# Performance work log

Measured on AMD Instinct MI355X. Metric: run time of the kernel, lower is better.

Reference implementation:

```python
import jax, jax.numpy as jnp
import numpy as np

DIL = 2  # dilation of the 3x3 neighborhood (hardcoded in the torch module)
# 8 non-center neighbor offsets of a dilated 3x3 kernel
_OFFSETS = [(-DIL, -DIL), (-DIL, 0), (-DIL, DIL),
            (0, -DIL),              (0, DIL),
            (DIL, -DIL), (DIL, 0),  (DIL, DIL)]


def setup_inputs() -> dict:
    key = jax.random.key(0)
    k1, k2 = jax.random.split(key)
    shape = (16, 1, 1024, 1024)
    y_true = jax.random.uniform(k1, shape, dtype=jnp.float32)
    y_pred = jax.random.uniform(k2, shape, dtype=jnp.float32)
    return {"y_true": y_true, "y_pred": y_pred}


def reference(y_true, y_pred):
    # --- BCE with torch's log clamp at -100 (reduction='none') ---
    log_p  = jnp.maximum(jnp.log(y_pred),   -100.0)
    log_1p = jnp.maximum(jnp.log1p(-y_pred), -100.0)
    a = -(y_true * log_p + (1.0 - y_true) * log_1p)

    # --- detached copy (y_pred.clone().detach()) ---
    sloss = jax.lax.stop_gradient(y_pred)

    # --- max |center - neighbor| over 8 dilated neighbors, zero-padded borders ---
    H, W = sloss.shape[2], sloss.shape[3]
    padded = jnp.pad(sloss, ((0, 0), (0, 0), (DIL, DIL), (DIL, DIL)))
    unfolded_weights = jnp.zeros_like(sloss)
    for dy, dx in _OFFSETS:
        nb = padded[:, :, DIL + dy:DIL + dy + H, DIL + dx:DIL + dx + W]
        unfolded_weights = jnp.maximum(unfolded_weights, jnp.abs(sloss - nb))

    # thred[thred < 0.5] = 0; loss1 uses thred BEFORE the >=0.5 -> 1 assignment
    thred = jnp.where(sloss >= 0.5, sloss, 0.0)
    loss = unfolded_weights * thred + a
    return loss.mean()
```

## Files before the change

kernel.cpp:

```cpp
#include <hip/hip_runtime.h>

#define HH 1024
#define WW 1024
#define NB 16
#define TR 8
#define SR (TR + 4)
#define NBLK (NB * (HH / TR))
#define NELEM ((long long)NB * HH * WW)

__device__ __forceinline__ void lds_win(const float* __restrict__ S, int row,
                                        int c0, bool ledge, bool redge, float w[8]) {
    const float* p = S + row * WW;
    float2 L = *(const float2*)(p + (ledge ? c0 : c0 - 2));
    float4 M = *(const float4*)(p + c0);
    float2 R = *(const float2*)(p + (redge ? c0 : c0 + 4));
    if (ledge) { L.x = 0.f; L.y = 0.f; }
    if (redge) { R.x = 0.f; R.y = 0.f; }
    w[0]=L.x; w[1]=L.y; w[2]=M.x; w[3]=M.y; w[4]=M.z; w[5]=M.w; w[6]=R.x; w[7]=R.y;
}

__global__ __launch_bounds__(512) void closs_main(const float* __restrict__ yt,
                                                  const float* __restrict__ yp,
                                                  float* __restrict__ partial) {
    __shared__ float S[SR * WW];

    const int bid   = blockIdx.x;
    const int img   = bid >> 7;
    const int tile  = bid & 127;
    const int y0    = tile * TR;
    const int tid   = threadIdx.x;
    const int lane  = tid & 255;
    const int rhalf = tid >> 8;
    const int c0    = lane << 2;

    const float* __restrict__ ybase = yp + (long long)img * (HH * WW);
    const float* __restrict__ tbase = yt + ((long long)img * HH + y0) * WW;

#pragma unroll
    for (int ii = 0; ii < 6; ++ii) {
        const int r  = (ii << 1) + rhalf;
        const int gy = y0 - 2 + r;
        float4 v = make_float4(0.f, 0.f, 0.f, 0.f);
        if (gy >= 0 && gy < HH)
            v = *(const float4*)(ybase + gy * WW + c0);
        *(float4*)&S[r * WW + c0] = v;
    }
    __syncthreads();

    const bool ledge = (lane == 0);
    const bool redge = (lane == 255);
    const int  kb    = rhalf << 2;

    float sum = 0.f;
#pragma unroll
    for (int k2 = 0; k2 < 4; ++k2) {
        const int k = kb + k2;
        float A[8], B[8], C[8];
        lds_win(S, k,     c0, ledge, redge, A);
        lds_win(S, k + 2, c0, ledge, redge, B);
        lds_win(S, k + 4, c0, ledge, redge, C);

        const float4 t4 = *(const float4*)(tbase + k * WW + c0);
        const float tt[4] = {t4.x, t4.y, t4.z, t4.w};

#pragma unroll
        for (int j = 0; j < 4; ++j) {
            const float c = B[j + 2];
            const float mxA = fmaxf(fmaxf(A[j], A[j + 2]), A[j + 4]);
            const float mxB = fmaxf(B[j], B[j + 4]);
            const float mxC = fmaxf(fmaxf(C[j], C[j + 2]), C[j + 4]);
            const float mx  = fmaxf(fmaxf(mxA, mxB), mxC);
            const float mnA = fminf(fminf(A[j], A[j + 2]), A[j + 4]);
            const float mnB = fminf(B[j], B[j + 4]);
            const float mnC = fminf(fminf(C[j], C[j + 2]), C[j + 4]);
            const float mn  = fminf(fminf(mnA, mnB), mnC);
            const float w   = fmaxf(mx - c, c - mn);

            const float lp  = fmaxf(__logf(c), -100.f);
            const float l1p = fmaxf(__logf(1.f - c), -100.f);
            const float th  = (c >= 0.5f) ? c : 0.f;
            sum += w * th - l1p - tt[j] * (lp - l1p);
        }
    }

    for (int o = 32; o > 0; o >>= 1) sum += __shfl_down(sum, o);
    __shared__ float wsum[8];
    if ((tid & 63) == 0) wsum[tid >> 6] = sum;
    __syncthreads();
    if (tid == 0) {
        float t = 0.f;
#pragma unroll
        for (int i = 0; i < 8; ++i) t += wsum[i];
        partial[bid] = t;
    }
}

__global__ __launch_bounds__(1024) void closs_reduce(const float* __restrict__ partial,
                                                     float* __restrict__ out) {
    const float2* p2 = (const float2*)partial;
    float2 v = p2[threadIdx.x];
    float s = v.x + v.y;
    for (int o = 32; o > 0; o >>= 1) s += __shfl_down(s, o);
    __shared__ float wsum[16];
    if ((threadIdx.x & 63) == 0) wsum[threadIdx.x >> 6] = s;
    __syncthreads();
    if (threadIdx.x == 0) {
        float t = 0.f;
#pragma unroll
        for (int i = 0; i < 16; ++i) t += wsum[i];
        out[0] = t * (1.0f / (float)NELEM);
    }
}

extern "C" void kernel_launch(void* const* d_in, const int* in_sizes, int n_in,
                              void* d_out, int out_size, void* d_ws, size_t ws_size,
                              hipStream_t stream) {
    const float* y_true = (const float*)d_in[0];
    const float* y_pred = (const float*)d_in[1];
    float* out = (float*)d_out;
    float* partial = (float*)d_ws;

    closs_main<<<NBLK, 512, 0, stream>>>(y_true, y_pred, partial);
    closs_reduce<<<1, 1024, 0, stream>>>(partial, out);
}
```

Baseline: 144.8 us.

## Double tile height and prefetch second-half rows during first-half compute

```diff
diff --git a/kernel.cpp b/kernel.cpp
--- a/kernel.cpp
+++ b/kernel.cpp
@@ -3,9 +3,9 @@
 #define HH 1024
 #define WW 1024
 #define NB 16
-#define TR 8
-#define SR (TR + 4)
-#define NBLK (NB * (HH / TR))
+#define TRB 16
+#define SRB 20
+#define NBLK (NB * (HH / TRB))
 #define NELEM ((long long)NB * HH * WW)
 
 __device__ __forceinline__ void lds_win(const float* __restrict__ S, int row,
@@ -19,15 +19,39 @@
     w[0]=L.x; w[1]=L.y; w[2]=M.x; w[3]=M.y; w[4]=M.z; w[5]=M.w; w[6]=R.x; w[7]=R.y;
 }
 
-__global__ __launch_bounds__(512) void closs_main(const float* __restrict__ yt,
-                                                  const float* __restrict__ yp,
-                                                  float* __restrict__ partial) {
-    __shared__ float S[SR * WW];
+__device__ __forceinline__ void row4(const float A[8], const float B[8],
+                                     const float C[8], const float4 t4,
+                                     float& sum) {
+    const float tt[4] = {t4.x, t4.y, t4.z, t4.w};
+#pragma unroll
+    for (int j = 0; j < 4; ++j) {
+        const float c = B[j + 2];
+        const float mxA = fmaxf(fmaxf(A[j], A[j + 2]), A[j + 4]);
+        const float mxB = fmaxf(B[j], B[j + 4]);
+        const float mxC = fmaxf(fmaxf(C[j], C[j + 2]), C[j + 4]);
+        const float mx  = fmaxf(fmaxf(mxA, mxB), mxC);
+        const float mnA = fminf(fminf(A[j], A[j + 2]), A[j + 4]);
+        const float mnB = fminf(B[j], B[j + 4]);
+        const float mnC = fminf(fminf(C[j], C[j + 2]), C[j + 4]);
+        const float mn  = fminf(fminf(mnA, mnB), mnC);
+        const float w   = fmaxf(mx - c, c - mn);
+
+        const float lp  = fmaxf(__logf(c), -100.f);
+        const float l1p = fmaxf(__logf(1.f - c), -100.f);
+        const float th  = (c >= 0.5f) ? c : 0.f;
+        sum += w * th - l1p - tt[j] * (lp - l1p);
+    }
+}
+
+__global__ __launch_bounds__(512, 4) void closs_main(const float* __restrict__ yt,
+                                                     const float* __restrict__ yp,
+                                                     float* __restrict__ partial) {
+    __shared__ float S[SRB * WW];
 
     const int bid   = blockIdx.x;
-    const int img   = bid >> 7;
-    const int tile  = bid & 127;
-    const int y0    = tile * TR;
+    const int img   = bid >> 6;
+    const int tile  = bid & 63;
+    const int y0    = tile << 4;
     const int tid   = threadIdx.x;
     const int lane  = tid & 255;
     const int rhalf = tid >> 8;
@@ -35,6 +59,9 @@
 
     const float* __restrict__ ybase = yp + (long long)img * (HH * WW);
     const float* __restrict__ tbase = yt + ((long long)img * HH + y0) * WW;
+
+    const bool ledge = (lane == 0);
+    const bool redge = (lane == 255);
 
 #pragma unroll
     for (int ii = 0; ii < 6; ++ii) {
@@ -47,59 +74,72 @@
     }
     __syncthreads();
 
-    const bool ledge = (lane == 0);
-    const bool redge = (lane == 255);
-    const int  kb    = rhalf << 2;
+    const int kb0 = rhalf << 2;
+
+    float4 T0[4];
+#pragma unroll
+    for (int q = 0; q < 4; ++q)
+        T0[q] = *(const float4*)(tbase + (kb0 + q) * WW + c0);
+
+    float4 P[4];
+#pragma unroll
+    for (int ii = 0; ii < 4; ++ii) {
+        const int r  = 12 + (ii << 1) + rhalf;
+        const int gy = y0 - 2 + r;
+        float4 v = make_float4(0.f, 0.f, 0.f, 0.f);
+        if (gy < HH)
+            v = *(const float4*)(ybase + gy * WW + c0);
+        P[ii] = v;
+    }
 
     float sum = 0.f;
 #pragma unroll
-    for (int k2 = 0; k2 < 4; ++k2) {
-        const int k = kb + k2;
+    for (int q = 0; q < 4; ++q) {
+        const int k = kb0 + q;
         float A[8], B[8], C[8];
         lds_win(S, k,     c0, ledge, redge, A);
         lds_win(S, k + 2, c0, ledge, redge, B);
         lds_win(S, k + 4, c0, ledge, redge, C);
+        row4(A, B, C, T0[q], sum);
+    }
 
-        const float4 t4 = *(const float4*)(tbase + k * WW + c0);
-        const float tt[4] = {t4.x, t4.y, t4.z, t4.w};
+    const int kb1 = 8 + kb0;
+    float4 T1[4];
+#pragma unroll
+    for (int q = 0; q < 4; ++q)
+        T1[q] = *(const float4*)(tbase + (kb1 + q) * WW + c0);
 
 #pragma unroll
-        for (int j = 0; j < 4; ++j) {
-            const float c = B[j + 2];
-            const float mxA = fmaxf(fmaxf(A[j], A[j + 2]), A[j + 4]);
-            const float mxB = fmaxf(B[j], B[j + 4]);
-            const float mxC = fmaxf(fmaxf(C[j], C[j + 2]), C[j + 4]);
-            const float mx  = fmaxf(fmaxf(mxA, mxB), mxC);
-            const float mnA = fminf(fminf(A[j], A[j + 2]), A[j + 4]);
-            const float mnB = fminf(B[j], B[j + 4]);
-            const float mnC = fminf(fminf(C[j], C[j + 2]), C[j + 4]);
-            const float mn  = fminf(fminf(mnA, mnB), mnC);
-            const float w   = fmaxf(mx - c, c - mn);
+    for (int ii = 0; ii < 4; ++ii) {
+        const int r = 12 + (ii << 1) + rhalf;
+        *(float4*)&S[r * WW + c0] = P[ii];
+    }
+    __syncthreads();
 
-            const float lp  = fmaxf(__logf(c), -100.f);
-            const float l1p = fmaxf(__logf(1.f - c), -100.f);
-            const float th  = (c >= 0.5f) ? c : 0.f;
-            sum += w * th - l1p - tt[j] * (lp - l1p);
-        }
+#pragma unroll
+    for (int q = 0; q < 4; ++q) {
+        const int k = kb1 + q;
+        float A[8], B[8], C[8];
+        lds_win(S, k,     c0, ledge, redge, A);
+        lds_win(S, k + 2, c0, ledge, redge, B);
+        lds_win(S, k + 4, c0, ledge, redge, C);
+        row4(A, B, C, T1[q], sum);
     }
 
     for (int o = 32; o > 0; o >>= 1) sum += __shfl_down(sum, o);
-    __shared__ float wsum[8];
-    if ((tid & 63) == 0) wsum[tid >> 6] = sum;
+    if ((tid & 63) == 0) S[tid >> 6] = sum;
     __syncthreads();
     if (tid == 0) {
         float t = 0.f;
 #pragma unroll
-        for (int i = 0; i < 8; ++i) t += wsum[i];
+        for (int i = 0; i < 8; ++i) t += S[i];
         partial[bid] = t;
     }
 }
 
 __global__ __launch_bounds__(1024) void closs_reduce(const float* __restrict__ partial,
                                                      float* __restrict__ out) {
-    const float2* p2 = (const float2*)partial;
-    float2 v = p2[threadIdx.x];
-    float s = v.x + v.y;
+    float s = partial[threadIdx.x];
     for (int o = 32; o > 0; o >>= 1) s += __shfl_down(s, o);
     __shared__ float wsum[16];
     if ((threadIdx.x & 63) == 0) wsum[threadIdx.x >> 6] = s;
```

After: 146.0 us. Within noise of the previous version (+0.8%).
